# Performance work log

Hardware: AMD Instinct MI355X
Metric: run time of the kernel (lower is better)

## Reference

```python
import jax, jax.numpy as jnp
import numpy as np

CUTOFFS = [0, 20000, 40000, 50000]
B, S, D = 2, 1024, 256

def setup_inputs() -> dict:
    key = jax.random.key(0)
    ks = jax.random.split(key, 6)
    x = jax.random.normal(ks[0], (B, S, D), dtype=jnp.float32)
    targets = jax.random.randint(ks[1], (B, S), 0, CUTOFFS[-1], dtype=jnp.int64)
    scale = 1.0 / np.sqrt(D)
    w0 = jax.random.normal(ks[2], (CUTOFFS[1] - CUTOFFS[0], D), dtype=jnp.float32) * scale
    w1 = jax.random.normal(ks[3], (CUTOFFS[2] - CUTOFFS[1], D), dtype=jnp.float32) * scale
    w2 = jax.random.normal(ks[4], (CUTOFFS[3] - CUTOFFS[2], D), dtype=jnp.float32) * scale
    b0 = jnp.zeros((CUTOFFS[1] - CUTOFFS[0],), dtype=jnp.float32)
    b1 = jnp.zeros((CUTOFFS[2] - CUTOFFS[1],), dtype=jnp.float32)
    b2 = jnp.zeros((CUTOFFS[3] - CUTOFFS[2],), dtype=jnp.float32)
    return {"x": x, "targets": targets, "w0": w0, "w1": w1, "w2": w2,
            "b0": b0, "b1": b1, "b2": b2}

def reference(x, targets, w0, w1, w2, b0, b1, b2):
    # Faithful to TF: for each cluster, compute dense logits for ALL tokens,
    # zero out positions whose target id is outside [l, r) (scatter_nd of the
    # boolean-masked logits into a zeros tensor == multiply by mask), concat
    # along vocab, then log_softmax over the full vocab.
    ws = [w0, w1, w2]
    bs = [b0, b1, b2]
    pieces = []
    for i in range(len(CUTOFFS) - 1):
        l, r = CUTOFFS[i], CUTOFFS[i + 1]
        mask = ((targets >= l) & (targets < r)).astype(x.dtype)[..., None]  # [B,S,1]
        logits = jnp.einsum('bsd,vd->bsv', x, ws[i]) + bs[i]               # [B,S,r-l]
        pieces.append(logits * mask)
    out = jnp.concatenate(pieces, axis=-1)  # [B,S,n_token]
    return jax.nn.log_softmax(out, axis=-1)
```

## Files before the change

### kernel.cpp

```cpp
#include <hip/hip_runtime.h>
#include <hip/hip_bf16.h>
#include <math.h>


typedef __attribute__((ext_vector_type(4))) float f32x4;
typedef __attribute__((ext_vector_type(8))) short bf16x8;
typedef __attribute__((ext_vector_type(4))) unsigned short u16x4;
typedef __attribute__((ext_vector_type(8))) unsigned short u16x8;

__device__ __forceinline__ unsigned int f2bf(float f) {
    union { float f; unsigned int u; } cv; cv.f = f;
    unsigned int u = cv.u + 0x7fffu + ((cv.u >> 16) & 1u);
    return u >> 16;
}
__device__ __forceinline__ float bf2f(unsigned short h) {
    union { unsigned int u; float f; } cv; cv.u = ((unsigned int)h) << 16;
    return cv.f;
}

__global__ __launch_bounds__(1024) void classify_kernel(
    const int* __restrict__ targets, int* cnt, int* lists,
    int n_tok, int c1, int c2) {
    __shared__ int lcnt[3];
    int tid = threadIdx.x;
    if (tid < 3) lcnt[tid] = 0;
    __syncthreads();
    for (int t = tid; t < n_tok; t += 1024) {
        int tgt = targets[t];
        int c = (tgt < c1) ? 0 : ((tgt < c2) ? 1 : 2);
        int pos = atomicAdd(&lcnt[c], 1);
        lists[c * n_tok + pos] = t;
    }
    __syncthreads();
    if (tid < 3) cnt[tid] = lcnt[tid];
}

__global__ __launch_bounds__(512) void pack_a_kernel(
    const float* __restrict__ x, const int* __restrict__ lists,
    const int* __restrict__ cnt, unsigned short* __restrict__ packA,
    int n_tok) {
    int it0 = (cnt[0] + 255) >> 8, it1 = (cnt[1] + 255) >> 8,
        it2 = (cnt[2] + 255) >> 8;
    int g0 = it0 * 16, g1 = it1 * 16, g2 = it2 * 16;
    int gb = blockIdx.x;
    int c, g, n, base;
    if (gb < g0)                { c = 0; g = gb;            n = cnt[0]; base = 0; }
    else if (gb < g0 + g1)      { c = 1; g = gb - g0;       n = cnt[1]; base = g0; }
    else if (gb < g0 + g1 + g2) { c = 2; g = gb - g0 - g1;  n = cnt[2]; base = g0 + g1; }
    else return;

    int tid = threadIdx.x;
    int k0 = tid >> 6, lane = tid & 63;
    int l15 = lane & 15, lg = lane >> 4;
    int pos = g * 16 + l15;
    int tok = (pos < n) ? lists[c * n_tok + pos] : -1;
    uint4 pk = make_uint4(0u, 0u, 0u, 0u);
    if (tok >= 0) {
        const float* src = x + (size_t)tok * 256 + k0 * 32 + lg * 8;
        float4 lo = *(const float4*)src;
        float4 hi = *(const float4*)(src + 4);
        pk.x = f2bf(lo.x) | (f2bf(lo.y) << 16);
        pk.y = f2bf(lo.z) | (f2bf(lo.w) << 16);
        pk.z = f2bf(hi.x) | (f2bf(hi.y) << 16);
        pk.w = f2bf(hi.z) | (f2bf(hi.w) << 16);
    }
    *(uint4*)(packA + ((size_t)(base + g) * 8 + k0) * 512 + lane * 8) = pk;
}

__global__ __launch_bounds__(256, 4) void gemm_ws_kernel(
    const unsigned short* __restrict__ packA,
    const float* __restrict__ w0, const float* __restrict__ w1,
    const float* __restrict__ w2,
    const float* __restrict__ b0, const float* __restrict__ b1,
    const float* __restrict__ b2,
    const int* __restrict__ lists, const int* __restrict__ cnt,
    int V0, int V1, int V2, int nv0, int nv1,
    unsigned short* __restrict__ lws, int lstride, int n_tok) {

    __shared__ __align__(16) unsigned char wlds[64 * 512];
    __shared__ int tok_lds[2048];

    int bid = blockIdx.x;
    int c, vt;
    if (bid < nv0)            { c = 0; vt = bid; }
    else if (bid < nv0 + nv1) { c = 1; vt = bid - nv0; }
    else                      { c = 2; vt = bid - nv0 - nv1; }

    const float* Wc; const float* Bc; int Vc;
    if (c == 0)      { Wc = w0; Bc = b0; Vc = V0; }
    else if (c == 1) { Wc = w1; Bc = b1; Vc = V1; }
    else             { Wc = w2; Bc = b2; Vc = V2; }

    int it0 = (cnt[0] + 255) >> 8, it1 = (cnt[1] + 255) >> 8;
    int baseg = (c == 0) ? 0 : ((c == 1) ? it0 * 16 : (it0 + it1) * 16);

    int n = cnt[c];
    int nIter = (n + 255) >> 8;
    int v0 = vt * 64;
    int tid = threadIdx.x;

    #pragma unroll
    for (int u0 = 0; u0 < 2; ++u0) {
        int u = u0 * 256 + tid;
        int row = u >> 3, seg = u & 7;
        int v = v0 + row;
        float4 f[8];
        if (v < Vc) {
            const float* src = Wc + (size_t)v * 256 + seg * 32;
            #pragma unroll
            for (int j = 0; j < 8; ++j) f[j] = *(const float4*)(src + j * 4);
        } else {
            #pragma unroll
            for (int j = 0; j < 8; ++j) f[j] = make_float4(0.f, 0.f, 0.f, 0.f);
        }
        unsigned fb = (unsigned)(((row >> 4) * 8 + seg) * 1024);
        int l15r = row & 15;
        #pragma unroll
        for (int j = 0; j < 4; ++j) {
            uint4 pk;
            pk.x = f2bf(f[2*j].x)   | (f2bf(f[2*j].y)   << 16);
            pk.y = f2bf(f[2*j].z)   | (f2bf(f[2*j].w)   << 16);
            pk.z = f2bf(f[2*j+1].x) | (f2bf(f[2*j+1].y) << 16);
            pk.w = f2bf(f[2*j+1].z) | (f2bf(f[2*j+1].w) << 16);
            *(uint4*)(wlds + fb + (j * 16 + l15r) * 16) = pk;
        }
    }
    for (int i = tid; i < nIter * 256; i += 256)
        tok_lds[i] = (i < n) ? lists[c * n_tok + i] : -1;
    __syncthreads();

    int lane = tid & 63;
    int wid  = tid >> 6;
    int lg = lane >> 4, l15 = lane & 15;
    const char* pA = (const char*)packA;

    float bv[4];
    #pragma unroll
    for (int nn = 0; nn < 4; ++nn) {
        int vl = v0 + nn * 16 + l15;
        bv[nn] = (vl < Vc) ? Bc[vl] : -__builtin_huge_valf();
    }

    for (int it = 0; it < nIter; ++it) {
        int tb = it * 256 + wid * 64;
        if (tb >= n) continue;
        const char* ga = pA + (size_t)(baseg + it * 16 + wid * 4) * 8192 + lane * 16;

        f32x4 acc[4][4];
        #pragma unroll
        for (int m = 0; m < 4; ++m)
            #pragma unroll
            for (int nn = 0; nn < 4; ++nn)
                acc[m][nn] = (f32x4){0.f, 0.f, 0.f, 0.f};

        #pragma unroll
        for (int k0 = 0; k0 < 8; ++k0) {
            bf16x8 a[4], b[4];
            #pragma unroll
            for (int m = 0; m < 4; ++m)
                a[m] = *(const bf16x8*)(ga + m * 8192 + k0 * 1024);
            #pragma unroll
            for (int nn = 0; nn < 4; ++nn)
                b[nn] = *(const bf16x8*)(wlds + (nn * 8 + k0) * 1024 + lane * 16);
            #pragma unroll
            for (int m = 0; m < 4; ++m)
                #pragma unroll
                for (int nn = 0; nn < 4; ++nn)
                    acc[m][nn] = __builtin_amdgcn_mfma_f32_16x16x32_bf16(
                        a[m], b[nn], acc[m][nn], 0, 0, 0);
        }

        #pragma unroll
        for (int m = 0; m < 4; ++m) {
            #pragma unroll
            for (int rr = 0; rr < 4; ++rr) {
                int tokid = tok_lds[tb + m * 16 + lg * 4 + rr];
                if (tokid >= 0) {
                    unsigned short* dst =
                        lws + (size_t)tokid * lstride + v0 + l15;
                    #pragma unroll
                    for (int nn = 0; nn < 4; ++nn)
                        dst[nn * 16] =
                            (unsigned short)f2bf(acc[m][nn][rr] + bv[nn]);
                }
            }
        }
    }
}

__global__ __launch_bounds__(256) void finalize_kernel(
    float* __restrict__ out, const unsigned short* __restrict__ lws,
    int lstride, const int* __restrict__ targets, int c1, int c2, int N) {
    __shared__ unsigned short srow[20000];
    __shared__ float sred[4];
    __shared__ float sL;

    int t = blockIdx.x;
    int tid = threadIdx.x;
    int tgt = targets[t];
    int l, r, V;
    if (tgt < c1)      { l = 0;  r = c1; V = c1; }
    else if (tgt < c2) { l = c1; r = c2; V = c2 - c1; }
    else               { l = c2; r = N;  V = N - c2; }

    const unsigned short* lrow = lws + (size_t)t * lstride;
    int Vp8 = (V + 7) & ~7;
    bool lds_ok = (Vp8 <= 20000);

    float s = 0.f;
    for (int i = tid * 8; i < Vp8; i += 2048) {
        u16x8 u = *(const u16x8*)(lrow + i);
        if (lds_ok) *(u16x8*)(srow + i) = u;
        s += __expf(bf2f(u.s0)) + __expf(bf2f(u.s1))
           + __expf(bf2f(u.s2)) + __expf(bf2f(u.s3))
           + __expf(bf2f(u.s4)) + __expf(bf2f(u.s5))
           + __expf(bf2f(u.s6)) + __expf(bf2f(u.s7));
    }
    s += __shfl_down(s, 32); s += __shfl_down(s, 16); s += __shfl_down(s, 8);
    s += __shfl_down(s, 4);  s += __shfl_down(s, 2);  s += __shfl_down(s, 1);
    if ((tid & 63) == 0) sred[tid >> 6] = s;
    __syncthreads();
    if (tid == 0)
        sL = logf(sred[0] + sred[1] + sred[2] + sred[3] + (float)(N - V));
    __syncthreads();
    float L = sL;

    float* orow = out + (size_t)t * N;
    f32x4 neg = (f32x4){-L, -L, -L, -L};
    for (int i4 = tid * 4; i4 < N; i4 += 1024) {
        f32x4 res;
        if (i4 >= l && i4 < r) {
            u16x4 u = lds_ok ? *(const u16x4*)(srow + (i4 - l))
                             : *(const u16x4*)(lrow + (i4 - l));
            res = (f32x4){bf2f(u.x) - L, bf2f(u.y) - L,
                          bf2f(u.z) - L, bf2f(u.w) - L};
        } else {
            res = neg;
        }
        __builtin_nontemporal_store(res, (f32x4*)(orow + i4));
    }
}

extern "C" void kernel_launch(void* const* d_in, const int* in_sizes, int n_in,
                              void* d_out, int out_size, void* d_ws, size_t ws_size,
                              hipStream_t stream) {
    const float* x       = (const float*)d_in[0];
    const int*   targets = (const int*)d_in[1];
    const float* w0      = (const float*)d_in[2];
    const float* w1      = (const float*)d_in[3];
    const float* w2      = (const float*)d_in[4];
    const float* b0      = (const float*)d_in[5];
    const float* b1      = (const float*)d_in[6];
    const float* b2      = (const float*)d_in[7];
    float* out = (float*)d_out;

    int n_tok = in_sizes[1];
    int V0 = in_sizes[5];
    int V1 = in_sizes[6];
    int V2 = in_sizes[7];
    int N  = V0 + V1 + V2;
    int c1 = V0, c2 = V0 + V1;
    int nv0 = (V0 + 63) >> 6, nv1 = (V1 + 63) >> 6, nv2 = (V2 + 63) >> 6;
    int maxV = V0 > V1 ? V0 : V1; if (V2 > maxV) maxV = V2;
    int lstride = ((maxV + 63) >> 6) << 6;

    int maxGroups = (((n_tok + 255) >> 8) + 3) << 4;

    char* ws = (char*)d_ws;
    size_t off = 0;
    int* cnt = (int*)(ws + off);      off += 256;
    int* lists = (int*)(ws + off);    off += (((size_t)3 * n_tok * 4 + 255) & ~(size_t)255);
    unsigned short* packA = (unsigned short*)(ws + off);
    off += (((size_t)maxGroups * 8192 + 255) & ~(size_t)255);
    unsigned short* lws = (unsigned short*)(ws + off);

    classify_kernel<<<1, 1024, 0, stream>>>(targets, cnt, lists, n_tok, c1, c2);

    pack_a_kernel<<<maxGroups, 512, 0, stream>>>(x, lists, cnt, packA, n_tok);

    gemm_ws_kernel<<<nv0 + nv1 + nv2, 256, 0, stream>>>(
        packA, w0, w1, w2, b0, b1, b2, lists, cnt,
        V0, V1, V2, nv0, nv1, lws, lstride, n_tok);

    finalize_kernel<<<n_tok, 256, 0, stream>>>(
        out, lws, lstride, targets, c1, c2, N);
}
```

Before: 147.8 us.

## Swap MFMA operands for vectorized logit stores and drop LDS row cache

The GEMM now feeds the weight tile as the A operand and the gathered activations as B. Each lane then holds four consecutive vocab entries for one token, so the bf16 logits can go out as 8-byte vector stores instead of scattered 2-byte stores, and biases are preloaded per lane to match. The finalize kernel drops its 40 KB LDS row copy and rereads the logit row from global memory (likely L2-resident), which frees LDS for more occupancy. The GEMM launch-bounds occupancy hint also drops from 4 to 3 blocks per CU, allowing more registers per thread.

New measurement: 151.5 us. +2.5%, slower.

```diff
diff --git a/kernel.cpp b/kernel.cpp
--- a/kernel.cpp
+++ b/kernel.cpp
@@ -67,7 +67,7 @@
     *(uint4*)(packA + ((size_t)(base + g) * 8 + k0) * 512 + lane * 8) = pk;
 }
 
-__global__ __launch_bounds__(256, 4) void gemm_ws_kernel(
+__global__ __launch_bounds__(256, 3) void gemm_ws_kernel(
     const unsigned short* __restrict__ packA,
     const float* __restrict__ w0, const float* __restrict__ w1,
     const float* __restrict__ w2,
@@ -134,11 +134,14 @@
     int lg = lane >> 4, l15 = lane & 15;
     const char* pA = (const char*)packA;
 
-    float bv[4];
+    float bvv[4][4];
     #pragma unroll
-    for (int nn = 0; nn < 4; ++nn) {
-        int vl = v0 + nn * 16 + l15;
-        bv[nn] = (vl < Vc) ? Bc[vl] : -__builtin_huge_valf();
+    for (int mv = 0; mv < 4; ++mv) {
+        int vbase = v0 + mv * 16 + lg * 4;
+        #pragma unroll
+        for (int r = 0; r < 4; ++r)
+            bvv[mv][r] = (vbase + r < Vc) ? Bc[vbase + r]
+                                          : -__builtin_huge_valf();
     }
 
     for (int it = 0; it < nIter; ++it) {
@@ -148,40 +151,42 @@
 
         f32x4 acc[4][4];
         #pragma unroll
-        for (int m = 0; m < 4; ++m)
-            #pragma unroll
-            for (int nn = 0; nn < 4; ++nn)
-                acc[m][nn] = (f32x4){0.f, 0.f, 0.f, 0.f};
+        for (int mv = 0; mv < 4; ++mv)
+            #pragma unroll
+            for (int nt = 0; nt < 4; ++nt)
+                acc[mv][nt] = (f32x4){0.f, 0.f, 0.f, 0.f};
 
         #pragma unroll
         for (int k0 = 0; k0 < 8; ++k0) {
-            bf16x8 a[4], b[4];
-            #pragma unroll
-            for (int m = 0; m < 4; ++m)
-                a[m] = *(const bf16x8*)(ga + m * 8192 + k0 * 1024);
-            #pragma unroll
-            for (int nn = 0; nn < 4; ++nn)
-                b[nn] = *(const bf16x8*)(wlds + (nn * 8 + k0) * 1024 + lane * 16);
-            #pragma unroll
-            for (int m = 0; m < 4; ++m)
+            bf16x8 w[4], xf[4];
+            #pragma unroll
+            for (int mv = 0; mv < 4; ++mv)
+                w[mv] = *(const bf16x8*)(wlds + (mv * 8 + k0) * 1024 + lane * 16);
+            #pragma unroll
+            for (int nt = 0; nt < 4; ++nt)
+                xf[nt] = *(const bf16x8*)(ga + nt * 8192 + k0 * 1024);
+            #pragma unroll
+            for (int mv = 0; mv < 4; ++mv)
                 #pragma unroll
-                for (int nn = 0; nn < 4; ++nn)
-                    acc[m][nn] = __builtin_amdgcn_mfma_f32_16x16x32_bf16(
-                        a[m], b[nn], acc[m][nn], 0, 0, 0);
-        }
-
-        #pragma unroll
-        for (int m = 0; m < 4; ++m) {
-            #pragma unroll
-            for (int rr = 0; rr < 4; ++rr) {
-                int tokid = tok_lds[tb + m * 16 + lg * 4 + rr];
-                if (tokid >= 0) {
-                    unsigned short* dst =
-                        lws + (size_t)tokid * lstride + v0 + l15;
-                    #pragma unroll
-                    for (int nn = 0; nn < 4; ++nn)
-                        dst[nn * 16] =
-                            (unsigned short)f2bf(acc[m][nn][rr] + bv[nn]);
+                for (int nt = 0; nt < 4; ++nt)
+                    acc[mv][nt] = __builtin_amdgcn_mfma_f32_16x16x32_bf16(
+                        w[mv], xf[nt], acc[mv][nt], 0, 0, 0);
+        }
+
+        #pragma unroll
+        for (int nt = 0; nt < 4; ++nt) {
+            int tokid = tok_lds[tb + nt * 16 + l15];
+            if (tokid >= 0) {
+                unsigned short* dst =
+                    lws + (size_t)tokid * lstride + v0 + lg * 4;
+                #pragma unroll
+                for (int mv = 0; mv < 4; ++mv) {
+                    u16x4 pk;
+                    pk.x = (unsigned short)f2bf(acc[mv][nt][0] + bvv[mv][0]);
+                    pk.y = (unsigned short)f2bf(acc[mv][nt][1] + bvv[mv][1]);
+                    pk.z = (unsigned short)f2bf(acc[mv][nt][2] + bvv[mv][2]);
+                    pk.w = (unsigned short)f2bf(acc[mv][nt][3] + bvv[mv][3]);
+                    *(u16x4*)(dst + mv * 16) = pk;
                 }
             }
         }
@@ -191,7 +196,6 @@
 __global__ __launch_bounds__(256) void finalize_kernel(
     float* __restrict__ out, const unsigned short* __restrict__ lws,
     int lstride, const int* __restrict__ targets, int c1, int c2, int N) {
-    __shared__ unsigned short srow[20000];
     __shared__ float sred[4];
     __shared__ float sL;
 
@@ -205,12 +209,10 @@
 
     const unsigned short* lrow = lws + (size_t)t * lstride;
     int Vp8 = (V + 7) & ~7;
-    bool lds_ok = (Vp8 <= 20000);
 
     float s = 0.f;
     for (int i = tid * 8; i < Vp8; i += 2048) {
         u16x8 u = *(const u16x8*)(lrow + i);
-        if (lds_ok) *(u16x8*)(srow + i) = u;
         s += __expf(bf2f(u.s0)) + __expf(bf2f(u.s1))
            + __expf(bf2f(u.s2)) + __expf(bf2f(u.s3))
            + __expf(bf2f(u.s4)) + __expf(bf2f(u.s5))
@@ -230,8 +232,7 @@
     for (int i4 = tid * 4; i4 < N; i4 += 1024) {
         f32x4 res;
         if (i4 >= l && i4 < r) {
-            u16x4 u = lds_ok ? *(const u16x4*)(srow + (i4 - l))
-                             : *(const u16x4*)(lrow + (i4 - l));
+            u16x4 u = *(const u16x4*)(lrow + (i4 - l));
             res = (f32x4){bf2f(u.x) - L, bf2f(u.y) - L,
                           bf2f(u.z) - L, bf2f(u.w) - L};
         } else {
```
